# Kernel tuning notes

Hardware: AMD Instinct MI355X
Metric: run time of the kernel (lower is better)

Reference implementation:

```python
import jax, jax.numpy as jnp
import numpy as np

B = 4096          # batch
IN = 4096         # in_features
OUT = 4096        # out_features
MASK_DENSITY = 0.1

def setup_inputs() -> dict:
    key = jax.random.key(0)
    k1, k2, k3, k4, k5 = jax.random.split(key, 5)
    x = jax.random.normal(k1, (B, IN), dtype=jnp.float32)
    # truncated-normal-ish init, std 0.1 (plain normal scaled is fine for a numeric baseline)
    weight = jax.random.normal(k2, (OUT, IN), dtype=jnp.float32) * 0.1
    bound = 1.0 / np.sqrt(IN)
    bias = jax.random.uniform(k3, (OUT,), dtype=jnp.float32, minval=-bound, maxval=bound)
    mask = jax.random.bernoulli(k4, MASK_DENSITY, (OUT, IN))  # bool, fixed sparsity pattern
    residual_connection = jax.random.randint(k5, (OUT,), 0, IN, dtype=jnp.int32)
    return {"x": x, "weight": weight, "bias": bias, "mask": mask,
            "residual_connection": residual_connection}

def reference(x, weight, bias, mask, residual_connection):
    # out = relu(x @ (mask * W)^T + b) + x[:, residual_connection]
    w_masked = jnp.where(mask, weight, 0.0)              # [OUT, IN]
    out = x @ w_masked.T + bias                          # [B, OUT]
    out = jax.nn.relu(out)
    out = jnp.take(x, residual_connection, axis=1) + out # gathered residual add
    return out
```

## Files before the change

### kernel.cpp

```cpp
#include <hip/hip_runtime.h>
#include <hip/hip_bf16.h>
#include <stdint.h>

#define B_ROWS 4096
#define IN_F   4096
#define OUT_F  4096

#define BM 256
#define BN 256
#define BK 64
#define NKT (IN_F / BK)

typedef float  f32x4  __attribute__((ext_vector_type(4)));
typedef short  bf16x8 __attribute__((ext_vector_type(8)));
typedef unsigned short u16x4 __attribute__((ext_vector_type(4)));

#define AS1 __attribute__((address_space(1)))
#define AS3 __attribute__((address_space(3)))

template<int N> struct IC { static constexpr int v = N; };

__device__ __forceinline__ uint16_t f2bf_rne(float f) {
    uint32_t u = __float_as_uint(f);
    uint32_t r = u + 0x7fffu + ((u >> 16) & 1u);
    return (uint16_t)(r >> 16);
}
__device__ __forceinline__ float bf2f(uint16_t h) {
    return __uint_as_float(((uint32_t)h) << 16);
}

__global__ __launch_bounds__(256) void prep_kernel(
    const float* __restrict__ x, uint16_t* __restrict__ xb, uint16_t* __restrict__ xbT,
    const float* __restrict__ w, const void* __restrict__ mraw, uint16_t* __restrict__ wb)
{
    const int tid = threadIdx.x;
    const int blk = blockIdx.x;

    if (blk < 4096) {
        __shared__ float t[64][65];
        const int r0 = (blk >> 6) * 64;
        const int c0 = (blk & 63) * 64;
        const int lr = tid >> 4;
        const int lc4 = (tid & 15) * 4;

#pragma unroll
        for (int p = 0; p < 4; ++p) {
            const int row = p * 16 + lr;
            float4 v = *(const float4*)(x + (size_t)(r0 + row) * IN_F + c0 + lc4);
            ushort4 o;
            o.x = f2bf_rne(v.x); o.y = f2bf_rne(v.y);
            o.z = f2bf_rne(v.z); o.w = f2bf_rne(v.w);
            *(ushort4*)(xb + (size_t)(r0 + row) * IN_F + c0 + lc4) = o;
            t[row][lc4 + 0] = v.x; t[row][lc4 + 1] = v.y;
            t[row][lc4 + 2] = v.z; t[row][lc4 + 3] = v.w;
        }
        __syncthreads();
#pragma unroll
        for (int p = 0; p < 4; ++p) {
            const int c = p * 16 + lr;
            ushort4 o;
            o.x = f2bf_rne(t[lc4 + 0][c]);
            o.y = f2bf_rne(t[lc4 + 1][c]);
            o.z = f2bf_rne(t[lc4 + 2][c]);
            o.w = f2bf_rne(t[lc4 + 3][c]);
            *(ushort4*)(xbT + (size_t)(c0 + c) * B_ROWS + r0 + lc4) = o;
        }
    } else {
        __shared__ int wflag[4];
        uint32_t mword = ((const uint32_t*)mraw)[tid];
        unsigned long long bal = __ballot((mword & 0xFFFFFF00u) != 0);
        if ((tid & 63) == 0) wflag[tid >> 6] = (bal != 0ull);
        __syncthreads();
        const int flag = wflag[0] | wflag[1] | wflag[2] | wflag[3];

#pragma unroll
        for (int it = 0; it < 4; ++it) {
            const size_t c = (size_t)(blk - 4096) + (size_t)it * 2048;
            const size_t e = c * 2048 + (size_t)tid * 8;
            float4 v0 = *(const float4*)(w + e);
            float4 v1 = *(const float4*)(w + e + 4);
            int m[8];
            if (flag) {
                uint2 mm = *(const uint2*)((const uint8_t*)mraw + e);
#pragma unroll
                for (int j = 0; j < 4; ++j) m[j]     = (mm.x >> (8 * j)) & 0xff;
#pragma unroll
                for (int j = 0; j < 4; ++j) m[4 + j] = (mm.y >> (8 * j)) & 0xff;
            } else {
                const int* mp = (const int*)mraw + e;
                int4 a = *(const int4*)mp;
                int4 b = *(const int4*)(mp + 4);
                m[0] = a.x; m[1] = a.y; m[2] = a.z; m[3] = a.w;
                m[4] = b.x; m[5] = b.y; m[6] = b.z; m[7] = b.w;
            }
            bf16x8 o;
            o[0] = m[0] ? (short)f2bf_rne(v0.x) : (short)0;
            o[1] = m[1] ? (short)f2bf_rne(v0.y) : (short)0;
            o[2] = m[2] ? (short)f2bf_rne(v0.z) : (short)0;
            o[3] = m[3] ? (short)f2bf_rne(v0.w) : (short)0;
            o[4] = m[4] ? (short)f2bf_rne(v1.x) : (short)0;
            o[5] = m[5] ? (short)f2bf_rne(v1.y) : (short)0;
            o[6] = m[6] ? (short)f2bf_rne(v1.z) : (short)0;
            o[7] = m[7] ? (short)f2bf_rne(v1.w) : (short)0;
            *(bf16x8*)(wb + e) = o;
        }
    }
}

#define DSR(dst, base, OFS) \
    asm volatile("ds_read_b128 %0, %1 offset:" #OFS : "=v"(dst) : "v"(base))
#define LDSOFF(p) ((uint32_t)(uintptr_t)(AS3 void*)(p))

__global__ __launch_bounds__(512, 2) void gemm_kernel(
    const uint16_t* __restrict__ xb, const uint16_t* __restrict__ wb,
    const uint16_t* __restrict__ xbT, const float* __restrict__ bias,
    const int* __restrict__ rc, float* __restrict__ out)
{
    __shared__ alignas(16) uint16_t Abuf[2][2][128 * BK];
    __shared__ alignas(16) uint16_t Bbuf[2][2][128 * BK];
    __shared__ float bias_s[BN];
    __shared__ int   rc_s[BN];

    const int tid = threadIdx.x;

    const int bid = blockIdx.x;
    const int wg  = (bid & 7) * 32 + (bid >> 3);
    const int row0 = (wg >> 4) * BM;
    const int col0 = (wg & 15) * BN;

    const int wave = tid >> 6, lane = tid & 63;
    const int wm = wave >> 2;
    const int wn = wave & 3;
    const int bh = wn >> 1;
    const int quad = lane >> 4, l16 = lane & 15;
    const int swr = (l16 & 7) << 3;
    const int e0  = (quad << 3) ^ swr;
    const uint32_t kd = (uint32_t)(((e0 ^ 32) - e0) * 2);

    const uint32_t aB0  = LDSOFF(&Abuf[0][wm][0]) + (uint32_t)((l16 * BK + e0) * 2);
    const uint32_t aB1  = LDSOFF(&Abuf[1][wm][0]) + (uint32_t)((l16 * BK + e0) * 2);
    const uint32_t bB0  = LDSOFF(&Bbuf[0][bh][0]) + (uint32_t)((((wn & 1) * 64 + l16) * BK + e0) * 2);
    const uint32_t bB1  = LDSOFF(&Bbuf[1][bh][0]) + (uint32_t)((((wn & 1) * 64 + l16) * BK + e0) * 2);
    const uint32_t aB0k = aB0 + kd, aB1k = aB1 + kd, bB0k = bB0 + kd, bB1k = bB1 + kd;

    const int srow = tid >> 3;
    const int ssw  = ((tid & 7) ^ (srow & 7)) << 3;
    const uint16_t* pA0 = xb + (size_t)(row0 + srow) * IN_F + ssw;
    const uint16_t* pB0 = wb + (size_t)(col0 + srow) * IN_F + ssw;
    const uint16_t* pA1 = pA0 + (size_t)128 * IN_F;
    const uint16_t* pB1 = pB0 + (size_t)128 * IN_F;

    auto stage = [&](const uint16_t* src, uint16_t* ldsdst, size_t ko) {
        __builtin_amdgcn_global_load_lds((const AS1 void*)(src + ko),
                                         (AS3 void*)(ldsdst + tid * 8), 16, 0, 0);
        __builtin_amdgcn_global_load_lds((const AS1 void*)(src + ko + (size_t)64 * IN_F),
                                         (AS3 void*)(ldsdst + tid * 8 + 4096), 16, 0, 0);
    };

    if (tid < BN) {
        __builtin_amdgcn_global_load_lds((const AS1 void*)(bias + col0 + tid),
                                         (AS3 void*)(bias_s + tid), 4, 0, 0);
        __builtin_amdgcn_global_load_lds((const AS1 void*)(rc + col0 + tid),
                                         (AS3 void*)(rc_s + tid), 4, 0, 0);
    }

    f32x4 acc[8][4];
#pragma unroll
    for (int mi = 0; mi < 8; ++mi)
#pragma unroll
        for (int ni = 0; ni < 4; ++ni)
            acc[mi][ni] = (f32x4){0.f, 0.f, 0.f, 0.f};

    stage(pA0, &Abuf[0][0][0], 0);
    stage(pA1, &Abuf[0][1][0], 0);
    stage(pB0, &Bbuf[0][0][0], 0);
    stage(pB1, &Bbuf[0][1][0], 0);
    asm volatile("s_waitcnt vmcnt(0)" ::: "memory");
    __builtin_amdgcn_s_barrier();
    __builtin_amdgcn_sched_barrier(0);

    bf16x8 a0p[4];
    DSR(a0p[0], aB0, 0);
    DSR(a0p[1], aB0, 2048);
    DSR(a0p[2], aB0, 4096);
    DSR(a0p[3], aB0, 6144);

#define LGKM(n) do { asm volatile("s_waitcnt lgkmcnt(" #n ")" ::: "memory"); \
                     __builtin_amdgcn_sched_barrier(0); } while (0)

    auto tile = [&](auto curc, int t) {
        constexpr int CUR = decltype(curc)::v;
        constexpr int NXT = CUR ^ 1;
        const uint32_t aB  = CUR ? aB1  : aB0;
        const uint32_t aBk = CUR ? aB1k : aB0k;
        const uint32_t bB  = CUR ? bB1  : bB0;
        const uint32_t bBk = CUR ? bB1k : bB0k;
        const uint32_t aN  = CUR ? aB0  : aB1;
        const size_t koff = (size_t)(t + 1) * BK;

        bf16x8 b[4], b2[4], a1[4], a2[4], a3[4];

        asm volatile("s_waitcnt vmcnt(0)" ::: "memory");
        __builtin_amdgcn_s_barrier();
        __builtin_amdgcn_sched_barrier(0);

        DSR(b[0], bB, 0); DSR(b[1], bB, 2048); DSR(b[2], bB, 4096); DSR(b[3], bB, 6144);
        DSR(a1[0], aB, 8192); DSR(a1[1], aB, 10240); DSR(a1[2], aB, 12288); DSR(a1[3], aB, 14336);
        stage(pA0, &Abuf[NXT][0][0], koff);
        stage(pA1, &Abuf[NXT][1][0], koff);

        LGKM(4);
        __builtin_amdgcn_s_setprio(1);
#pragma unroll
        for (int m = 0; m < 4; ++m)
#pragma unroll
            for (int ni = 0; ni < 4; ++ni)
                acc[m][ni] = __builtin_amdgcn_mfma_f32_16x16x32_bf16(a0p[m], b[ni], acc[m][ni], 0, 0, 0);
        __builtin_amdgcn_s_setprio(0);

        DSR(a2[0], aBk, 0); DSR(a2[1], aBk, 2048); DSR(a2[2], aBk, 4096); DSR(a2[3], aBk, 6144);
        stage(pB0, &Bbuf[NXT][0][0], koff);
        stage(pB1, &Bbuf[NXT][1][0], koff);

        LGKM(4);
        __builtin_amdgcn_s_setprio(1);
#pragma unroll
        for (int m = 0; m < 4; ++m)
#pragma unroll
            for (int ni = 0; ni < 4; ++ni)
                acc[4 + m][ni] = __builtin_amdgcn_mfma_f32_16x16x32_bf16(a1[m], b[ni], acc[4 + m][ni], 0, 0, 0);
        __builtin_amdgcn_s_setprio(0);

        DSR(b2[0], bBk, 0); DSR(b2[1], bBk, 2048); DSR(b2[2], bBk, 4096); DSR(b2[3], bBk, 6144);
        DSR(a3[0], aBk, 8192); DSR(a3[1], aBk, 10240); DSR(a3[2], aBk, 12288); DSR(a3[3], aBk, 14336);

        asm volatile("s_waitcnt vmcnt(4)" ::: "memory");
        __builtin_amdgcn_s_barrier();
        __builtin_amdgcn_sched_barrier(0);

        LGKM(4);
        __builtin_amdgcn_s_setprio(1);
#pragma unroll
        for (int m = 0; m < 4; ++m)
#pragma unroll
            for (int ni = 0; ni < 4; ++ni)
                acc[m][ni] = __builtin_amdgcn_mfma_f32_16x16x32_bf16(a2[m], b2[ni], acc[m][ni], 0, 0, 0);
        __builtin_amdgcn_s_setprio(0);

        DSR(a0p[0], aN, 0); DSR(a0p[1], aN, 2048); DSR(a0p[2], aN, 4096); DSR(a0p[3], aN, 6144);

        LGKM(4);
        __builtin_amdgcn_s_setprio(1);
#pragma unroll
        for (int m = 0; m < 4; ++m)
#pragma unroll
            for (int ni = 0; ni < 4; ++ni)
                acc[4 + m][ni] = __builtin_amdgcn_mfma_f32_16x16x32_bf16(a3[m], b2[ni], acc[4 + m][ni], 0, 0, 0);
        __builtin_amdgcn_s_setprio(0);
    };

    for (int tt = 0; tt < NKT; tt += 2) {
        tile(IC<0>{}, tt);
        tile(IC<1>{}, tt + 1);
    }
#undef LGKM

#pragma unroll
    for (int ni = 0; ni < 4; ++ni) {
        const int lcol = wn * 64 + ni * 16 + l16;
        const int gcol = col0 + lcol;
        const float bv = bias_s[lcol];
        const int   rv = rc_s[lcol];
#pragma unroll
        for (int mi = 0; mi < 8; ++mi) {
            const int grow0 = row0 + wm * 128 + mi * 16 + quad * 4;
            u16x4 xq = *(const u16x4*)(xbT + (size_t)rv * B_ROWS + grow0);
#pragma unroll
            for (int r = 0; r < 4; ++r) {
                float v = fmaxf(acc[mi][ni][r] + bv, 0.0f) + bf2f(xq[r]);
                out[(size_t)(grow0 + r) * OUT_F + gcol] = v;
            }
        }
    }
}

extern "C" void kernel_launch(void* const* d_in, const int* in_sizes, int n_in,
                              void* d_out, int out_size, void* d_ws, size_t ws_size,
                              hipStream_t stream) {
    const float* x    = (const float*)d_in[0];
    const float* w    = (const float*)d_in[1];
    const float* bias = (const float*)d_in[2];
    const void*  mask = (const void*)d_in[3];
    const int*   rc   = (const int*)d_in[4];
    float* out = (float*)d_out;

    uint16_t* xb   = (uint16_t*)d_ws;
    uint16_t* wb   = xb  + (size_t)B_ROWS * IN_F;
    uint16_t* xbT  = wb  + (size_t)OUT_F * IN_F;

    prep_kernel<<<4096 + 2048, 256, 0, stream>>>(x, xb, xbT, w, mask, wb);

    gemm_kernel<<<dim3((B_ROWS / BM) * (OUT_F / BN)), dim3(512), 0, stream>>>(
        xb, wb, xbT, bias, rc, out);
}
```

Before: 348.7 us.

## Load A operand fragments directly from global into registers, bypassing LDS

The A (activation) tile is no longer staged through LDS. Each wave now issues global_load_dwordx4 straight into its MFMA operand registers with per-row pointers, while B keeps its LDS double buffer. This removes the LDS traffic and footprint for A and reorganises the vmcnt/lgkmcnt waits and barriers around the new load order. In exchange, A loads become uncoalesced per-wave reads that are duplicated across the four wn waves, and MFMA latency hiding now depends on global load latency.

```diff
diff --git a/kernel.cpp b/kernel.cpp
--- a/kernel.cpp
+++ b/kernel.cpp
@@ -108,15 +108,17 @@
 }
 
 #define DSR(dst, base, OFS) \
-    asm volatile("ds_read_b128 %0, %1 offset:" #OFS : "=v"(dst) : "v"(base))
+    asm volatile("ds_read_b128 %0, %1 offset:" #OFS : "=&v"(dst) : "v"(base))
+#define GLD(dst, p, OFS) \
+    asm volatile("global_load_dwordx4 %0, %1, off offset:" #OFS : "=&v"(dst) : "v"(p))
 #define LDSOFF(p) ((uint32_t)(uintptr_t)(AS3 void*)(p))
+#define SB() __builtin_amdgcn_sched_barrier(0)
 
 __global__ __launch_bounds__(512, 2) void gemm_kernel(
     const uint16_t* __restrict__ xb, const uint16_t* __restrict__ wb,
     const uint16_t* __restrict__ xbT, const float* __restrict__ bias,
     const int* __restrict__ rc, float* __restrict__ out)
 {
-    __shared__ alignas(16) uint16_t Abuf[2][2][128 * BK];
     __shared__ alignas(16) uint16_t Bbuf[2][2][128 * BK];
     __shared__ float bias_s[BN];
     __shared__ int   rc_s[BN];
@@ -137,17 +139,13 @@
     const int e0  = (quad << 3) ^ swr;
     const uint32_t kd = (uint32_t)(((e0 ^ 32) - e0) * 2);
 
-    const uint32_t aB0  = LDSOFF(&Abuf[0][wm][0]) + (uint32_t)((l16 * BK + e0) * 2);
-    const uint32_t aB1  = LDSOFF(&Abuf[1][wm][0]) + (uint32_t)((l16 * BK + e0) * 2);
     const uint32_t bB0  = LDSOFF(&Bbuf[0][bh][0]) + (uint32_t)((((wn & 1) * 64 + l16) * BK + e0) * 2);
     const uint32_t bB1  = LDSOFF(&Bbuf[1][bh][0]) + (uint32_t)((((wn & 1) * 64 + l16) * BK + e0) * 2);
-    const uint32_t aB0k = aB0 + kd, aB1k = aB1 + kd, bB0k = bB0 + kd, bB1k = bB1 + kd;
+    const uint32_t bB0k = bB0 + kd, bB1k = bB1 + kd;
 
     const int srow = tid >> 3;
     const int ssw  = ((tid & 7) ^ (srow & 7)) << 3;
-    const uint16_t* pA0 = xb + (size_t)(row0 + srow) * IN_F + ssw;
     const uint16_t* pB0 = wb + (size_t)(col0 + srow) * IN_F + ssw;
-    const uint16_t* pA1 = pA0 + (size_t)128 * IN_F;
     const uint16_t* pB1 = pB0 + (size_t)128 * IN_F;
 
     auto stage = [&](const uint16_t* src, uint16_t* ldsdst, size_t ko) {
@@ -157,72 +155,68 @@
                                          (AS3 void*)(ldsdst + tid * 8 + 4096), 16, 0, 0);
     };
 
+    const uint16_t* paB = xb + (size_t)(row0 + wm * 128 + l16) * IN_F + quad * 8;
+    const uint16_t* pa0 = paB;
+    const uint16_t* pa1 = paB + (size_t)16 * IN_F;
+    const uint16_t* pa2 = paB + (size_t)32 * IN_F;
+    const uint16_t* pa3 = paB + (size_t)48 * IN_F;
+    const uint16_t* pa4 = paB + (size_t)64 * IN_F;
+    const uint16_t* pa5 = paB + (size_t)80 * IN_F;
+    const uint16_t* pa6 = paB + (size_t)96 * IN_F;
+    const uint16_t* pa7 = paB + (size_t)112 * IN_F;
+
+    f32x4 acc[8][4];
+#pragma unroll
+    for (int mi = 0; mi < 8; ++mi)
+#pragma unroll
+        for (int ni = 0; ni < 4; ++ni)
+            acc[mi][ni] = (f32x4){0.f, 0.f, 0.f, 0.f};
+
+    bf16x8 a0[4], a1[4], a2[4], a3[4], b[4], b2[4];
+
     if (tid < BN) {
         __builtin_amdgcn_global_load_lds((const AS1 void*)(bias + col0 + tid),
                                          (AS3 void*)(bias_s + tid), 4, 0, 0);
         __builtin_amdgcn_global_load_lds((const AS1 void*)(rc + col0 + tid),
                                          (AS3 void*)(rc_s + tid), 4, 0, 0);
     }
-
-    f32x4 acc[8][4];
-#pragma unroll
-    for (int mi = 0; mi < 8; ++mi)
-#pragma unroll
-        for (int ni = 0; ni < 4; ++ni)
-            acc[mi][ni] = (f32x4){0.f, 0.f, 0.f, 0.f};
-
-    stage(pA0, &Abuf[0][0][0], 0);
-    stage(pA1, &Abuf[0][1][0], 0);
     stage(pB0, &Bbuf[0][0][0], 0);
     stage(pB1, &Bbuf[0][1][0], 0);
-    asm volatile("s_waitcnt vmcnt(0)" ::: "memory");
+    SB();
+    GLD(a0[0], pa0, 0); GLD(a0[1], pa1, 0); GLD(a0[2], pa2, 0); GLD(a0[3], pa3, 0);
+    asm volatile("s_waitcnt vmcnt(4)" ::: "memory");
+    SB();
     __builtin_amdgcn_s_barrier();
-    __builtin_amdgcn_sched_barrier(0);
-
-    bf16x8 a0p[4];
-    DSR(a0p[0], aB0, 0);
-    DSR(a0p[1], aB0, 2048);
-    DSR(a0p[2], aB0, 4096);
-    DSR(a0p[3], aB0, 6144);
-
-#define LGKM(n) do { asm volatile("s_waitcnt lgkmcnt(" #n ")" ::: "memory"); \
-                     __builtin_amdgcn_sched_barrier(0); } while (0)
+
+#define WAITV(n) do { asm volatile("s_waitcnt vmcnt(" #n ")" ::: "memory"); SB(); } while (0)
+#define WAITL(n) do { asm volatile("s_waitcnt lgkmcnt(" #n ")" ::: "memory"); SB(); } while (0)
 
     auto tile = [&](auto curc, int t) {
         constexpr int CUR = decltype(curc)::v;
         constexpr int NXT = CUR ^ 1;
-        const uint32_t aB  = CUR ? aB1  : aB0;
-        const uint32_t aBk = CUR ? aB1k : aB0k;
         const uint32_t bB  = CUR ? bB1  : bB0;
         const uint32_t bBk = CUR ? bB1k : bB0k;
-        const uint32_t aN  = CUR ? aB0  : aB1;
         const size_t koff = (size_t)(t + 1) * BK;
 
-        bf16x8 b[4], b2[4], a1[4], a2[4], a3[4];
-
-        asm volatile("s_waitcnt vmcnt(0)" ::: "memory");
-        __builtin_amdgcn_s_barrier();
-        __builtin_amdgcn_sched_barrier(0);
-
-        DSR(b[0], bB, 0); DSR(b[1], bB, 2048); DSR(b[2], bB, 4096); DSR(b[3], bB, 6144);
-        DSR(a1[0], aB, 8192); DSR(a1[1], aB, 10240); DSR(a1[2], aB, 12288); DSR(a1[3], aB, 14336);
-        stage(pA0, &Abuf[NXT][0][0], koff);
-        stage(pA1, &Abuf[NXT][1][0], koff);
-
-        LGKM(4);
-        __builtin_amdgcn_s_setprio(1);
-#pragma unroll
-        for (int m = 0; m < 4; ++m)
-#pragma unroll
-            for (int ni = 0; ni < 4; ++ni)
-                acc[m][ni] = __builtin_amdgcn_mfma_f32_16x16x32_bf16(a0p[m], b[ni], acc[m][ni], 0, 0, 0);
-        __builtin_amdgcn_s_setprio(0);
-
-        DSR(a2[0], aBk, 0); DSR(a2[1], aBk, 2048); DSR(a2[2], aBk, 4096); DSR(a2[3], aBk, 6144);
+        DSR(b[0],  bB,  0); DSR(b[1],  bB,  2048); DSR(b[2],  bB,  4096); DSR(b[3],  bB,  6144);
+        DSR(b2[0], bBk, 0); DSR(b2[1], bBk, 2048); DSR(b2[2], bBk, 4096); DSR(b2[3], bBk, 6144);
+        GLD(a1[0], pa4, 0); GLD(a1[1], pa5, 0); GLD(a1[2], pa6, 0); GLD(a1[3], pa7, 0);
+        SB();
         stage(pB0, &Bbuf[NXT][0][0], koff);
         stage(pB1, &Bbuf[NXT][1][0], koff);
 
-        LGKM(4);
+        WAITV(8);
+        WAITL(4);
+        __builtin_amdgcn_s_setprio(1);
+#pragma unroll
+        for (int m = 0; m < 4; ++m)
+#pragma unroll
+            for (int ni = 0; ni < 4; ++ni)
+                acc[m][ni] = __builtin_amdgcn_mfma_f32_16x16x32_bf16(a0[m], b[ni], acc[m][ni], 0, 0, 0);
+        __builtin_amdgcn_s_setprio(0);
+
+        GLD(a2[0], pa0, 64); GLD(a2[1], pa1, 64); GLD(a2[2], pa2, 64); GLD(a2[3], pa3, 64);
+        WAITV(8);
         __builtin_amdgcn_s_setprio(1);
 #pragma unroll
         for (int m = 0; m < 4; ++m)
@@ -231,14 +225,9 @@
                 acc[4 + m][ni] = __builtin_amdgcn_mfma_f32_16x16x32_bf16(a1[m], b[ni], acc[4 + m][ni], 0, 0, 0);
         __builtin_amdgcn_s_setprio(0);
 
-        DSR(b2[0], bBk, 0); DSR(b2[1], bBk, 2048); DSR(b2[2], bBk, 4096); DSR(b2[3], bBk, 6144);
-        DSR(a3[0], aBk, 8192); DSR(a3[1], aBk, 10240); DSR(a3[2], aBk, 12288); DSR(a3[3], aBk, 14336);
-
-        asm volatile("s_waitcnt vmcnt(4)" ::: "memory");
-        __builtin_amdgcn_s_barrier();
-        __builtin_amdgcn_sched_barrier(0);
-
-        LGKM(4);
+        GLD(a3[0], pa4, 64); GLD(a3[1], pa5, 64); GLD(a3[2], pa6, 64); GLD(a3[3], pa7, 64);
+        WAITV(4);
+        WAITL(0);
         __builtin_amdgcn_s_setprio(1);
 #pragma unroll
         for (int m = 0; m < 4; ++m)
@@ -247,9 +236,10 @@
                 acc[m][ni] = __builtin_amdgcn_mfma_f32_16x16x32_bf16(a2[m], b2[ni], acc[m][ni], 0, 0, 0);
         __builtin_amdgcn_s_setprio(0);
 
-        DSR(a0p[0], aN, 0); DSR(a0p[1], aN, 2048); DSR(a0p[2], aN, 4096); DSR(a0p[3], aN, 6144);
-
-        LGKM(4);
+        pa0 += BK; pa1 += BK; pa2 += BK; pa3 += BK;
+        pa4 += BK; pa5 += BK; pa6 += BK; pa7 += BK;
+        GLD(a0[0], pa0, 0); GLD(a0[1], pa1, 0); GLD(a0[2], pa2, 0); GLD(a0[3], pa3, 0);
+        WAITV(4);
         __builtin_amdgcn_s_setprio(1);
 #pragma unroll
         for (int m = 0; m < 4; ++m)
@@ -260,10 +250,18 @@
     };
 
     for (int tt = 0; tt < NKT; tt += 2) {
+        __builtin_amdgcn_s_barrier();
+        SB();
         tile(IC<0>{}, tt);
+        __builtin_amdgcn_s_barrier();
+        SB();
         tile(IC<1>{}, tt + 1);
     }
-#undef LGKM
+#undef WAITV
+#undef WAITL
+
+    asm volatile("s_waitcnt vmcnt(0) lgkmcnt(0)" ::: "memory");
+    SB();
 
 #pragma unroll
     for (int ni = 0; ni < 4; ++ni) {
```

Result: slower. 512.0 us (+46.8%).
